# Kernel tuning notes

Hardware: AMD Instinct MI355X
Metric: run time of the kernel (lower is better)

The kernel has to match this reference:

```python
import jax, jax.numpy as jnp
import numpy as np

N_QUBITS = 4
N_LAYERS = 2
BATCH = 524288


def _apply_1q(state, U, axis):
    # state: [B, 2,2,2,2]; U: [2,2] (shared) or [B,2,2] (per-sample); axis = wire index + 1
    s = jnp.moveaxis(state, axis, -1)
    if U.ndim == 3:
        s = jnp.einsum('bij,b...j->b...i', U, s)
    else:
        s = jnp.einsum('ij,...j->...i', U, s)
    return jnp.moveaxis(s, -1, axis)


def _apply_cz(state, a, b):
    # diagonal CZ: flip sign where both qubits are |1>
    sign = jnp.array([[1.0, 1.0], [1.0, -1.0]], dtype=state.dtype)
    shape = [1] * state.ndim
    shape[a] = 2
    shape[b] = 2
    return state * sign.reshape(shape)


def _quantum_expval(feats, w):
    # feats: [B, n_qubits] angles; w: [n_layers, n_qubits, 3] Rot params
    B = feats.shape[0]
    state = jnp.zeros((B,) + (2,) * N_QUBITS, jnp.complex64)
    state = state.at[(slice(None),) + (0,) * N_QUBITS].set(1.0)
    # per-sample RY embedding
    for i in range(N_QUBITS):
        c = jnp.cos(feats[:, i] * 0.5)
        s = jnp.sin(feats[:, i] * 0.5)
        U = jnp.stack([jnp.stack([c, -s], -1), jnp.stack([s, c], -1)], -2).astype(jnp.complex64)
        state = _apply_1q(state, U, i + 1)
    # variational layers: Rot(phi,theta,omega) = RZ(omega) RY(theta) RZ(phi), then CZ chain
    for l in range(N_LAYERS):
        for i in range(N_QUBITS):
            phi, theta, omega = w[l, i, 0], w[l, i, 1], w[l, i, 2]
            ct = jnp.cos(theta * 0.5)
            st = jnp.sin(theta * 0.5)
            U = jnp.stack([
                jnp.stack([jnp.exp(-0.5j * (phi + omega)) * ct, -jnp.exp(0.5j * (phi - omega)) * st]),
                jnp.stack([jnp.exp(-0.5j * (phi - omega)) * st, jnp.exp(0.5j * (phi + omega)) * ct]),
            ]).astype(jnp.complex64)
            state = _apply_1q(state, U, i + 1)
        for i in range(N_QUBITS - 1):
            state = _apply_cz(state, i + 1, i + 2)
    probs = jnp.square(jnp.abs(state))
    p = probs.sum(axis=tuple(range(2, N_QUBITS + 1)))  # marginal of wire 0 -> [B, 2]
    return (p[:, 0] - p[:, 1]).astype(jnp.float32)  # <Z_0>


def setup_inputs() -> dict:
    key = jax.random.key(0)
    ks = jax.random.split(key, 12)
    f = jnp.float32
    return {
        'text': jax.random.normal(ks[0], (BATCH, 16), f),
        'image': jax.random.normal(ks[1], (BATCH, 48), f),
        'tW1': jax.random.normal(ks[2], (16, 32), f) * 0.25,
        'tb1': jnp.zeros((32,), f),
        'tW2': jax.random.normal(ks[3], (32, N_QUBITS), f) * 0.18,
        'tb2': jnp.zeros((N_QUBITS,), f),
        'iW1': jax.random.normal(ks[4], (48, 64), f) * 0.14,
        'ib1': jnp.zeros((64,), f),
        'iW2': jax.random.normal(ks[5], (64, N_QUBITS), f) * 0.125,
        'ib2': jnp.zeros((N_QUBITS,), f),
        'qweights': jax.random.normal(ks[6], (N_LAYERS, N_QUBITS, 3), f),
        'cW1': jax.random.normal(ks[7], (1, 16), f),
        'cb1': jnp.zeros((16,), f),
        'cW2': jax.random.normal(ks[8], (16, 2), f) * 0.25,
        'cb2': jnp.zeros((2,), f),
    }


def reference(text, image, tW1, tb1, tW2, tb2, iW1, ib1, iW2, ib2, qweights, cW1, cb1, cW2, cb2):
    tf = jax.nn.relu(text @ tW1 + tb1) @ tW2 + tb2      # [B, 4]
    imf = jax.nn.relu(image @ iW1 + ib1) @ iW2 + ib2    # [B, 4]
    feats = (tf + imf) * 0.5                             # [B, 4]
    q = _quantum_expval(feats, qweights)                 # [B]
    h = jax.nn.relu(q[:, None] @ cW1 + cb1)              # [B, 16]
    return h @ cW2 + cb2                                 # [B, 2]
```

## Files before the change

### kernel.cpp

```cpp
#include <hip/hip_runtime.h>
#include <math.h>

#define NQ 4
#define NL 2

__global__ void qnn_precompute_A(const float* __restrict__ qw, float* __restrict__ A)
{
    __shared__ float Mre[16][16];
    __shared__ float Mim[16][16];
    int t = threadIdx.x;
    if (t < 16) {
        int j = t;
        float re[16], im[16];
        for (int b = 0; b < 16; ++b) { re[b] = (b == j) ? 1.f : 0.f; im[b] = 0.f; }
        for (int l = 0; l < NL; ++l) {
            for (int i = 0; i < NQ; ++i) {
                float phi   = qw[(l*NQ + i)*3 + 0];
                float theta = qw[(l*NQ + i)*3 + 1];
                float omega = qw[(l*NQ + i)*3 + 2];
                float ct, st; sincosf(0.5f*theta, &st, &ct);
                float ap = 0.5f*(phi + omega);
                float am = 0.5f*(phi - omega);
                float cap, sap, cam, sam;
                sincosf(ap, &sap, &cap);
                sincosf(am, &sam, &cam);
                float u00r =  cap*ct, u00i = -sap*ct;
                float u01r = -cam*st, u01i = -sam*st;
                float u10r =  cam*st, u10i = -sam*st;
                float u11r =  cap*ct, u11i =  sap*ct;
                int mask = 1 << (3 - i);
                for (int b = 0; b < 16; ++b) {
                    if (b & mask) continue;
                    int b1 = b | mask;
                    float a0r = re[b],  a0i = im[b];
                    float a1r = re[b1], a1i = im[b1];
                    re[b]  = u00r*a0r - u00i*a0i + u01r*a1r - u01i*a1i;
                    im[b]  = u00r*a0i + u00i*a0r + u01r*a1i + u01i*a1r;
                    re[b1] = u10r*a0r - u10i*a0i + u11r*a1r - u11i*a1i;
                    im[b1] = u10r*a0i + u10i*a0r + u11r*a1i + u11i*a1r;
                }
            }
            for (int b = 0; b < 16; ++b) {
                float sgn = 1.f;
                if ((b & 0xC) == 0xC) sgn = -sgn;
                if ((b & 0x6) == 0x6) sgn = -sgn;
                if ((b & 0x3) == 0x3) sgn = -sgn;
                re[b] *= sgn; im[b] *= sgn;
            }
        }
        for (int b = 0; b < 16; ++b) { Mre[j][b] = re[b]; Mim[j][b] = im[b]; }
    }
    __syncthreads();
    {
        int j = t >> 4, k = t & 15;
        float s = 0.f;
        #pragma unroll
        for (int b = 0; b < 16; ++b) {
            float sg = (b & 8) ? -1.f : 1.f;
            s += sg * (Mre[j][b]*Mre[k][b] + Mim[j][b]*Mim[k][b]);
        }
        A[j*16 + k] = s;
    }
}

__global__ __launch_bounds__(256, 8) void qnn_main(
    const float* __restrict__ text, const float* __restrict__ image,
    const float* __restrict__ tW1, const float* __restrict__ tb1,
    const float* __restrict__ tW2, const float* __restrict__ tb2,
    const float* __restrict__ iW1, const float* __restrict__ ib1,
    const float* __restrict__ iW2, const float* __restrict__ ib2,
    const float* __restrict__ A,
    const float* __restrict__ cW1, const float* __restrict__ cb1,
    const float* __restrict__ cW2, const float* __restrict__ cb2,
    float* __restrict__ out, int B)
{
    int b = blockIdx.x * blockDim.x + threadIdx.x;
    if (b >= B) return;

    float acc[4];
    #pragma unroll
    for (int o = 0; o < 4; ++o) acc[o] = tb2[o] + ib2[o];

    {
        float h1[32];
        #pragma unroll
        for (int j = 0; j < 32; ++j) h1[j] = tb1[j];
        const float4* t4 = (const float4*)(text + (size_t)b * 16);
        #pragma unroll
        for (int k4 = 0; k4 < 4; ++k4) {
            float4 v = t4[k4];
            const float* w = tW1 + k4 * 4 * 32;
            #pragma unroll
            for (int j = 0; j < 32; ++j) h1[j] = fmaf(v.x, w[j],      h1[j]);
            #pragma unroll
            for (int j = 0; j < 32; ++j) h1[j] = fmaf(v.y, w[32 + j], h1[j]);
            #pragma unroll
            for (int j = 0; j < 32; ++j) h1[j] = fmaf(v.z, w[64 + j], h1[j]);
            #pragma unroll
            for (int j = 0; j < 32; ++j) h1[j] = fmaf(v.w, w[96 + j], h1[j]);
        }
        #pragma unroll
        for (int j = 0; j < 32; ++j) {
            float r = fmaxf(h1[j], 0.f);
            const float* w2 = tW2 + j * 4;
            #pragma unroll
            for (int o = 0; o < 4; ++o) acc[o] = fmaf(r, w2[o], acc[o]);
        }
    }

    #pragma unroll 1
    for (int cc = 0; cc < 64; cc += 32) {
        float h2[32];
        #pragma unroll
        for (int j = 0; j < 32; ++j) h2[j] = ib1[cc + j];
        const float4* i4 = (const float4*)(image + (size_t)b * 48);
        #pragma unroll 2
        for (int k4 = 0; k4 < 12; ++k4) {
            float4 v = i4[k4];
            const float* w = iW1 + k4 * 4 * 64 + cc;
            #pragma unroll
            for (int j = 0; j < 32; ++j) h2[j] = fmaf(v.x, w[j],       h2[j]);
            #pragma unroll
            for (int j = 0; j < 32; ++j) h2[j] = fmaf(v.y, w[64 + j],  h2[j]);
            #pragma unroll
            for (int j = 0; j < 32; ++j) h2[j] = fmaf(v.z, w[128 + j], h2[j]);
            #pragma unroll
            for (int j = 0; j < 32; ++j) h2[j] = fmaf(v.w, w[192 + j], h2[j]);
        }
        #pragma unroll
        for (int j = 0; j < 32; ++j) {
            float r = fmaxf(h2[j], 0.f);
            const float* w2 = iW2 + (cc + j) * 4;
            #pragma unroll
            for (int o = 0; o < 4; ++o) acc[o] = fmaf(r, w2[o], acc[o]);
        }
    }

    float c[4], s[4];
    #pragma unroll
    for (int i = 0; i < 4; ++i) {
        float f = acc[i] * 0.25f;
        __sincosf(f, &s[i], &c[i]);
    }
    float p01[4] = { c[0]*c[1], c[0]*s[1], s[0]*c[1], s[0]*s[1] };
    float p23[4] = { c[2]*c[3], c[2]*s[3], s[2]*c[3], s[2]*s[3] };
    float psi[16];
    #pragma unroll
    for (int x = 0; x < 4; ++x)
        #pragma unroll
        for (int y = 0; y < 4; ++y)
            psi[x*4+y] = p01[x] * p23[y];

    float q = 0.f;
    #pragma unroll
    for (int j = 0; j < 16; ++j) {
        float row = 0.f;
        #pragma unroll
        for (int k = 0; k < 16; ++k) row = fmaf(A[j*16+k], psi[k], row);
        q = fmaf(psi[j], row, q);
    }

    float o0 = cb2[0], o1 = cb2[1];
    #pragma unroll
    for (int j = 0; j < 16; ++j) {
        float h = fmaxf(fmaf(q, cW1[j], cb1[j]), 0.f);
        o0 = fmaf(h, cW2[j*2+0], o0);
        o1 = fmaf(h, cW2[j*2+1], o1);
    }
    float2* o2 = (float2*)out;
    o2[b] = make_float2(o0, o1);
}

extern "C" void kernel_launch(void* const* d_in, const int* in_sizes, int n_in,
                              void* d_out, int out_size, void* d_ws, size_t ws_size,
                              hipStream_t stream)
{
    const float* text  = (const float*)d_in[0];
    const float* image = (const float*)d_in[1];
    const float* tW1   = (const float*)d_in[2];
    const float* tb1   = (const float*)d_in[3];
    const float* tW2   = (const float*)d_in[4];
    const float* tb2   = (const float*)d_in[5];
    const float* iW1   = (const float*)d_in[6];
    const float* ib1   = (const float*)d_in[7];
    const float* iW2   = (const float*)d_in[8];
    const float* ib2   = (const float*)d_in[9];
    const float* qw    = (const float*)d_in[10];
    const float* cW1   = (const float*)d_in[11];
    const float* cb1   = (const float*)d_in[12];
    const float* cW2   = (const float*)d_in[13];
    const float* cb2   = (const float*)d_in[14];

    float* A = (float*)d_ws;
    int B = in_sizes[0] / 16;

    qnn_precompute_A<<<1, 256, 0, stream>>>(qw, A);

    int block = 256;
    int grid = (B + block - 1) / block;
    qnn_main<<<grid, block, 0, stream>>>(
        text, image, tW1, tb1, tW2, tb2, iW1, ib1, iW2, ib2,
        A, cW1, cb1, cW2, cb2, (float*)d_out, B);
}
```

Measured before the change: 277.4 us.

## Compute MLP first layers with bf16 split-precision MFMA instead of scalar FMAs

Replaces the per-thread scalar FMA loops for the text and image first layers with 16x16x32 bf16 MFMA instructions. A three-term hi/lo bf16 split keeps close to fp32 accuracy. Each wave handles 64 samples in four 16-row tiles, reduces the second-layer projections across lanes with shuffles, and stages the features in shared memory before the per-sample quantum and classifier tail. The change is meant to remove the heavy scalar FMA cost. In exchange it adds split/convert overhead, shuffles, a block barrier and a lower occupancy hint.

```diff
diff --git a/kernel.cpp b/kernel.cpp
--- a/kernel.cpp
+++ b/kernel.cpp
@@ -3,6 +3,26 @@
 
 #define NQ 4
 #define NL 2
+
+typedef __attribute__((ext_vector_type(8))) short short8v;
+typedef __attribute__((ext_vector_type(4))) float f32x4;
+
+__device__ inline unsigned short f2bf(float x){
+    unsigned u = __float_as_uint(x);
+    u += 0x7FFFu + ((u >> 16) & 1u);
+    return (unsigned short)(u >> 16);
+}
+__device__ inline float bf2f(unsigned short h){
+    return __uint_as_float(((unsigned)h) << 16);
+}
+__device__ inline void split8(const float* x, short8v& hi, short8v& lo){
+    #pragma unroll
+    for (int e = 0; e < 8; ++e){
+        unsigned short h = f2bf(x[e]);
+        hi[e] = (short)h;
+        lo[e] = (short)f2bf(x[e] - bf2f(h));
+    }
+}
 
 __global__ void qnn_precompute_A(const float* __restrict__ qw, float* __restrict__ A)
 {
@@ -63,7 +83,7 @@
     }
 }
 
-__global__ __launch_bounds__(256, 8) void qnn_main(
+__global__ __launch_bounds__(256, 3) void qnn_main(
     const float* __restrict__ text, const float* __restrict__ image,
     const float* __restrict__ tW1, const float* __restrict__ tb1,
     const float* __restrict__ tW2, const float* __restrict__ tb2,
@@ -74,101 +94,186 @@
     const float* __restrict__ cW2, const float* __restrict__ cb2,
     float* __restrict__ out, int B)
 {
-    int b = blockIdx.x * blockDim.x + threadIdx.x;
-    if (b >= B) return;
-
-    float acc[4];
-    #pragma unroll
-    for (int o = 0; o < 4; ++o) acc[o] = tb2[o] + ib2[o];
-
-    {
-        float h1[32];
-        #pragma unroll
-        for (int j = 0; j < 32; ++j) h1[j] = tb1[j];
-        const float4* t4 = (const float4*)(text + (size_t)b * 16);
-        #pragma unroll
-        for (int k4 = 0; k4 < 4; ++k4) {
-            float4 v = t4[k4];
-            const float* w = tW1 + k4 * 4 * 32;
-            #pragma unroll
-            for (int j = 0; j < 32; ++j) h1[j] = fmaf(v.x, w[j],      h1[j]);
-            #pragma unroll
-            for (int j = 0; j < 32; ++j) h1[j] = fmaf(v.y, w[32 + j], h1[j]);
-            #pragma unroll
-            for (int j = 0; j < 32; ++j) h1[j] = fmaf(v.z, w[64 + j], h1[j]);
-            #pragma unroll
-            for (int j = 0; j < 32; ++j) h1[j] = fmaf(v.w, w[96 + j], h1[j]);
-        }
-        #pragma unroll
-        for (int j = 0; j < 32; ++j) {
-            float r = fmaxf(h1[j], 0.f);
-            const float* w2 = tW2 + j * 4;
-            #pragma unroll
-            for (int o = 0; o < 4; ++o) acc[o] = fmaf(r, w2[o], acc[o]);
-        }
-    }
+    __shared__ float4 feats[256];
+    const int t    = threadIdx.x;
+    const int lane = t & 63;
+    const int wv   = t >> 6;
+    const int g    = lane >> 4;
+    const int c    = lane & 15;
+    const long long blockBase = (long long)blockIdx.x * 256;
+
+    short8v Bih[4][2], Bil[4][2];
+    #pragma unroll
+    for (int nt = 0; nt < 4; ++nt)
+        #pragma unroll
+        for (int ks = 0; ks < 2; ++ks){
+            float x[8];
+            #pragma unroll
+            for (int e = 0; e < 8; ++e){
+                int k = ks*32 + 8*g + e;
+                x[e] = (k < 48) ? iW1[k*64 + nt*16 + c] : 0.f;
+            }
+            split8(x, Bih[nt][ks], Bil[nt][ks]);
+        }
+    short8v Bth[2], Btl[2];
+    #pragma unroll
+    for (int nt = 0; nt < 2; ++nt){
+        float x[8];
+        #pragma unroll
+        for (int e = 0; e < 8; ++e){
+            int k = 8*g + e;
+            x[e] = (k < 16) ? tW1[k*32 + nt*16 + c] : 0.f;
+        }
+        split8(x, Bth[nt], Btl[nt]);
+    }
+    float ib1c[4], tb1c[2];
+    #pragma unroll
+    for (int nt = 0; nt < 4; ++nt) ib1c[nt] = ib1[nt*16 + c];
+    #pragma unroll
+    for (int nt = 0; nt < 2; ++nt) tb1c[nt] = tb1[nt*16 + c];
 
     #pragma unroll 1
-    for (int cc = 0; cc < 64; cc += 32) {
-        float h2[32];
-        #pragma unroll
-        for (int j = 0; j < 32; ++j) h2[j] = ib1[cc + j];
-        const float4* i4 = (const float4*)(image + (size_t)b * 48);
-        #pragma unroll 2
-        for (int k4 = 0; k4 < 12; ++k4) {
-            float4 v = i4[k4];
-            const float* w = iW1 + k4 * 4 * 64 + cc;
-            #pragma unroll
-            for (int j = 0; j < 32; ++j) h2[j] = fmaf(v.x, w[j],       h2[j]);
-            #pragma unroll
-            for (int j = 0; j < 32; ++j) h2[j] = fmaf(v.y, w[64 + j],  h2[j]);
-            #pragma unroll
-            for (int j = 0; j < 32; ++j) h2[j] = fmaf(v.z, w[128 + j], h2[j]);
-            #pragma unroll
-            for (int j = 0; j < 32; ++j) h2[j] = fmaf(v.w, w[192 + j], h2[j]);
-        }
-        #pragma unroll
-        for (int j = 0; j < 32; ++j) {
-            float r = fmaxf(h2[j], 0.f);
-            const float* w2 = iW2 + (cc + j) * 4;
-            #pragma unroll
-            for (int o = 0; o < 4; ++o) acc[o] = fmaf(r, w2[o], acc[o]);
-        }
-    }
-
-    float c[4], s[4];
-    #pragma unroll
-    for (int i = 0; i < 4; ++i) {
-        float f = acc[i] * 0.25f;
-        __sincosf(f, &s[i], &c[i]);
-    }
-    float p01[4] = { c[0]*c[1], c[0]*s[1], s[0]*c[1], s[0]*s[1] };
-    float p23[4] = { c[2]*c[3], c[2]*s[3], s[2]*c[3], s[2]*s[3] };
-    float psi[16];
-    #pragma unroll
-    for (int x = 0; x < 4; ++x)
-        #pragma unroll
-        for (int y = 0; y < 4; ++y)
-            psi[x*4+y] = p01[x] * p23[y];
-
-    float q = 0.f;
-    #pragma unroll
-    for (int j = 0; j < 16; ++j) {
-        float row = 0.f;
-        #pragma unroll
-        for (int k = 0; k < 16; ++k) row = fmaf(A[j*16+k], psi[k], row);
-        q = fmaf(psi[j], row, q);
-    }
-
-    float o0 = cb2[0], o1 = cb2[1];
-    #pragma unroll
-    for (int j = 0; j < 16; ++j) {
-        float h = fmaxf(fmaf(q, cW1[j], cb1[j]), 0.f);
-        o0 = fmaf(h, cW2[j*2+0], o0);
-        o1 = fmaf(h, cW2[j*2+1], o1);
-    }
-    float2* o2 = (float2*)out;
-    o2[b] = make_float2(o0, o1);
+    for (int ms = 0; ms < 4; ++ms){
+        long long m = blockBase + wv*64 + ms*16 + c;
+        if (m >= B) m = B - 1;
+        const float* irow = image + m*48;
+        const float* trow = text  + m*16;
+
+        short8v Aih[2], Ail[2], Ath, Atl;
+        {
+            float x[8];
+            float4 v0 = *(const float4*)(irow + 8*g);
+            float4 v1 = *(const float4*)(irow + 8*g + 4);
+            x[0]=v0.x; x[1]=v0.y; x[2]=v0.z; x[3]=v0.w;
+            x[4]=v1.x; x[5]=v1.y; x[6]=v1.z; x[7]=v1.w;
+            split8(x, Aih[0], Ail[0]);
+
+            float xi[8], xt[8];
+            #pragma unroll
+            for (int e = 0; e < 8; ++e){ xi[e] = 0.f; xt[e] = 0.f; }
+            if (g < 2){
+                float4 v2 = *(const float4*)(irow + 32 + 8*g);
+                float4 v3 = *(const float4*)(irow + 32 + 8*g + 4);
+                xi[0]=v2.x; xi[1]=v2.y; xi[2]=v2.z; xi[3]=v2.w;
+                xi[4]=v3.x; xi[5]=v3.y; xi[6]=v3.z; xi[7]=v3.w;
+                float4 t0 = *(const float4*)(trow + 8*g);
+                float4 t1 = *(const float4*)(trow + 8*g + 4);
+                xt[0]=t0.x; xt[1]=t0.y; xt[2]=t0.z; xt[3]=t0.w;
+                xt[4]=t1.x; xt[5]=t1.y; xt[6]=t1.z; xt[7]=t1.w;
+            }
+            split8(xi, Aih[1], Ail[1]);
+            split8(xt, Ath, Atl);
+        }
+
+        float po[4][4];
+        #pragma unroll
+        for (int r = 0; r < 4; ++r)
+            #pragma unroll
+            for (int o = 0; o < 4; ++o) po[r][o] = 0.f;
+
+        #pragma unroll
+        for (int nt = 0; nt < 4; ++nt){
+            f32x4 cc = { ib1c[nt], ib1c[nt], ib1c[nt], ib1c[nt] };
+            #pragma unroll
+            for (int ks = 0; ks < 2; ++ks){
+                cc = __builtin_amdgcn_mfma_f32_16x16x32_bf16(Aih[ks], Bih[nt][ks], cc, 0, 0, 0);
+                cc = __builtin_amdgcn_mfma_f32_16x16x32_bf16(Aih[ks], Bil[nt][ks], cc, 0, 0, 0);
+                cc = __builtin_amdgcn_mfma_f32_16x16x32_bf16(Ail[ks], Bih[nt][ks], cc, 0, 0, 0);
+            }
+            const float4 w2 = *(const float4*)(iW2 + (nt*16 + c)*4);
+            #pragma unroll
+            for (int r = 0; r < 4; ++r){
+                float h = fmaxf(cc[r], 0.f);
+                po[r][0] = fmaf(h, w2.x, po[r][0]);
+                po[r][1] = fmaf(h, w2.y, po[r][1]);
+                po[r][2] = fmaf(h, w2.z, po[r][2]);
+                po[r][3] = fmaf(h, w2.w, po[r][3]);
+            }
+        }
+        #pragma unroll
+        for (int nt = 0; nt < 2; ++nt){
+            f32x4 cc = { tb1c[nt], tb1c[nt], tb1c[nt], tb1c[nt] };
+            cc = __builtin_amdgcn_mfma_f32_16x16x32_bf16(Ath, Bth[nt], cc, 0, 0, 0);
+            cc = __builtin_amdgcn_mfma_f32_16x16x32_bf16(Ath, Btl[nt], cc, 0, 0, 0);
+            cc = __builtin_amdgcn_mfma_f32_16x16x32_bf16(Atl, Bth[nt], cc, 0, 0, 0);
+            const float4 w2 = *(const float4*)(tW2 + (nt*16 + c)*4);
+            #pragma unroll
+            for (int r = 0; r < 4; ++r){
+                float h = fmaxf(cc[r], 0.f);
+                po[r][0] = fmaf(h, w2.x, po[r][0]);
+                po[r][1] = fmaf(h, w2.y, po[r][1]);
+                po[r][2] = fmaf(h, w2.z, po[r][2]);
+                po[r][3] = fmaf(h, w2.w, po[r][3]);
+            }
+        }
+
+        #pragma unroll
+        for (int r = 0; r < 4; ++r)
+            #pragma unroll
+            for (int o = 0; o < 4; ++o){
+                float v = po[r][o];
+                v += __shfl_xor(v, 1);
+                v += __shfl_xor(v, 2);
+                v += __shfl_xor(v, 4);
+                v += __shfl_xor(v, 8);
+                po[r][o] = v;
+            }
+
+        if (c < 4){
+            float4 v;
+            if      (c == 0) v = make_float4(po[0][0], po[0][1], po[0][2], po[0][3]);
+            else if (c == 1) v = make_float4(po[1][0], po[1][1], po[1][2], po[1][3]);
+            else if (c == 2) v = make_float4(po[2][0], po[2][1], po[2][2], po[2][3]);
+            else             v = make_float4(po[3][0], po[3][1], po[3][2], po[3][3]);
+            feats[wv*64 + ms*16 + 4*g + c] = v;
+        }
+    }
+
+    __syncthreads();
+
+    long long samp = blockBase + t;
+    if (samp < B){
+        float4 f4 = feats[t];
+        float acc[4];
+        acc[0] = tb2[0] + ib2[0] + f4.x;
+        acc[1] = tb2[1] + ib2[1] + f4.y;
+        acc[2] = tb2[2] + ib2[2] + f4.z;
+        acc[3] = tb2[3] + ib2[3] + f4.w;
+
+        float cth[4], sth[4];
+        #pragma unroll
+        for (int i = 0; i < 4; ++i){
+            float f = acc[i] * 0.25f;
+            __sincosf(f, &sth[i], &cth[i]);
+        }
+        float p01[4] = { cth[0]*cth[1], cth[0]*sth[1], sth[0]*cth[1], sth[0]*sth[1] };
+        float p23[4] = { cth[2]*cth[3], cth[2]*sth[3], sth[2]*cth[3], sth[2]*sth[3] };
+        float psi[16];
+        #pragma unroll
+        for (int x = 0; x < 4; ++x)
+            #pragma unroll
+            for (int y = 0; y < 4; ++y)
+                psi[x*4+y] = p01[x] * p23[y];
+
+        float q = 0.f;
+        #pragma unroll
+        for (int j = 0; j < 16; ++j){
+            float row = 0.f;
+            #pragma unroll
+            for (int k = 0; k < 16; ++k) row = fmaf(A[j*16+k], psi[k], row);
+            q = fmaf(psi[j], row, q);
+        }
+
+        float o0 = cb2[0], o1 = cb2[1];
+        #pragma unroll
+        for (int j = 0; j < 16; ++j){
+            float h = fmaxf(fmaf(q, cW1[j], cb1[j]), 0.f);
+            o0 = fmaf(h, cW2[j*2+0], o0);
+            o1 = fmaf(h, cW2[j*2+1], o1);
+        }
+        float2* o2 = (float2*)out;
+        o2[samp] = make_float2(o0, o1);
+    }
 }
 
 extern "C" void kernel_launch(void* const* d_in, const int* in_sizes, int n_in,
```

After: 287.9 us. 3.8% more time.
